# Kernel tuning notes

Hardware: AMD Instinct MI355X
Metric: run time of the kernel (lower is better)

## Reference

```python
import jax, jax.numpy as jnp
import numpy as np

ALPHA = 0.2  # LeakyReLU negative slope
EPS = 1e-16


def setup_inputs() -> dict:
    key = jax.random.key(0)
    k0, k1, k2, k3 = jax.random.split(key, 4)
    N, E, F_in, F_out, HEADS = 50000, 1600000, 256, 128, 4
    H = jax.random.normal(k0, (N, F_in), dtype=jnp.float32)
    edge_index = jax.random.randint(k1, (2, E), 0, N)  # row0=src, row1=dst
    # Xavier-ish scaled params
    W = jax.random.normal(k2, (HEADS, F_out, F_in), dtype=jnp.float32) * (1.0 / np.sqrt(F_in))
    a = jax.random.normal(k3, (HEADS, 2 * F_out), dtype=jnp.float32) * 0.1
    bias = jnp.zeros((F_out,), dtype=jnp.float32)
    return {"H": H, "edge_index": edge_index, "W": W, "a": a, "bias": bias}


def reference(H, edge_index, W, a, bias):
    """GAT layer: per-head edge attention + segment softmax over src + SpMM, mean over heads.

    H: [N, F_in]; edge_index: [2, E]; W: [heads, F_out, F_in]; a: [heads, 2*F_out]; bias: [F_out]
    Note: a(concat(h_src, h_dst)) == h_src @ a[:F_out] + h_dst @ a[F_out:], so we compute the
    two per-node scores once on nodes instead of materializing the E x 2*F_out concat.
    """
    N = H.shape[0]
    heads, F_out, _ = W.shape
    src, dst = edge_index[0], edge_index[1]
    outs = []
    for h in range(heads):
        Ht = H @ W[h].T                      # [N, F_out]
        s_src = Ht @ a[h, :F_out]            # [N]
        s_dst = Ht @ a[h, F_out:]            # [N]
        e = s_src[src] + s_dst[dst]          # [E]
        e = jnp.where(e > 0, e, ALPHA * e)   # LeakyReLU
        # segment softmax over src nodes (matches scatter amax + scatter_add)
        e_max = jax.ops.segment_max(e, src, num_segments=N)    # [N], -inf for isolated nodes
        e_exp = jnp.exp(e - e_max[src])                         # [E]
        denom = jax.ops.segment_sum(e_exp, src, num_segments=N) # [N]
        attn = e_exp / (denom[src] + EPS)                       # [E]
        # sparse.mm(attention, Ht): out[i] = sum_{(i,j) in E} attn_ij * Ht[j]
        out = jax.ops.segment_sum(attn[:, None] * Ht[dst], src, num_segments=N)  # [N, F_out]
        outs.append(out)
    final = jnp.mean(jnp.stack(outs, axis=0), axis=0) + bias
    return final
```

## Files before the change

kernel.cpp:

```cpp
#include <hip/hip_runtime.h>

#define ALPHA 0.2f
#define EPS 1e-16f

static constexpr int F_IN = 256;
static constexpr int F_OUT = 128;
static constexpr int HEADS = 4;
static constexpr int COLS = HEADS * F_OUT;

typedef __bf16 bf16x8 __attribute__((ext_vector_type(8)));
typedef float f32x4 __attribute__((ext_vector_type(4)));

static __device__ __forceinline__ unsigned short f2bf(float f) {
  unsigned int u = __float_as_uint(f);
  unsigned int r = (u + 0x7FFFu + ((u >> 16) & 1u)) >> 16;
  return (unsigned short)r;
}
static __device__ __forceinline__ float bf_lo(unsigned int u) {
  return __uint_as_float(u << 16);
}
static __device__ __forceinline__ float bf_hi(unsigned int u) {
  return __uint_as_float(u & 0xFFFF0000u);
}

__global__ __launch_bounds__(256) void k_wprep(const float* __restrict__ W,
                                               const float* __restrict__ a,
                                               unsigned short* __restrict__ Wb,
                                               float* __restrict__ u) {
  if (blockIdx.x < 128) {
    const int i = blockIdx.x * 256 + threadIdx.x;
    const float4 v = ((const float4*)W)[i];
    ((ushort4*)Wb)[i] = make_ushort4(f2bf(v.x), f2bf(v.y), f2bf(v.z), f2bf(v.w));
  } else {
    const int b = blockIdx.x - 128;
    const int h = b >> 1, dual = b & 1;
    const int k = threadIdx.x;
    float s = 0.f;
    for (int f = 0; f < F_OUT; ++f)
      s = fmaf(a[h * 2 * F_OUT + dual * F_OUT + f], W[((size_t)h * F_OUT + f) * F_IN + k], s);
    u[b * F_IN + k] = s;
  }
}

__global__ __launch_bounds__(256) void k_pre(const float4* __restrict__ H4,
    const float* __restrict__ u, unsigned short* __restrict__ Hb,
    float4* __restrict__ ssrc4, unsigned char* __restrict__ rec, int N, int CB,
    const int* __restrict__ src, int* __restrict__ cnt,
    unsigned short* __restrict__ rank, int E) {
  if ((int)blockIdx.x >= CB) {
    int i = (blockIdx.x - CB) * 256 + threadIdx.x;
    const int stride = 1024 * 256;
    for (; i < E; i += stride) rank[i] = (unsigned short)atomicAdd(&cnt[src[i]], 1);
    return;
  }
  const int wv = threadIdx.x >> 6, lane = threadIdx.x & 63;
  const int n = ((int)blockIdx.x << 2) + wv;
  if (n >= N) return;
  const float4 hv = H4[(size_t)n * 64 + lane];
  *((ushort4*)(Hb + (size_t)n * F_IN) + lane) =
      make_ushort4(f2bf(hv.x), f2bf(hv.y), f2bf(hv.z), f2bf(hv.w));
  float p[8];
#pragma unroll
  for (int c = 0; c < 8; ++c) {
    const float4 uv = *(const float4*)&u[c * F_IN + (lane << 2)];
    p[c] = fmaf(hv.x, uv.x, fmaf(hv.y, uv.y, fmaf(hv.z, uv.z, hv.w * uv.w)));
  }
#pragma unroll
  for (int c = 0; c < 8; ++c)
#pragma unroll
    for (int m = 1; m < 64; m <<= 1) p[c] += __shfl_xor(p[c], m);
  if (lane == 0) {
    ssrc4[n] = make_float4(p[0], p[2], p[4], p[6]);
    *(float4*)&rec[(size_t)n * 32] = make_float4(p[1], p[3], p[5], p[7]);
  }
}

__global__ __launch_bounds__(256) void k_gemm_q(const unsigned short* __restrict__ A,
                                                const unsigned short* __restrict__ B,
                                                unsigned char* __restrict__ Hq,
                                                unsigned char* __restrict__ rec, int N) {
  __shared__ __bf16 As[128][40];
  __shared__ __bf16 Bs[128][40];
  const int T = gridDim.x;
  const int q8 = T >> 3, r8 = T & 7;
  const int xcd = blockIdx.x & 7, ii = blockIdx.x >> 3;
  const int gp = (xcd < r8) ? xcd * (q8 + 1) + ii
                            : r8 * (q8 + 1) + (xcd - r8) * q8 + ii;
  const int by = gp >> 2;
  const int bx = gp & 3;
  const int t = threadIdx.x;
  const int w = t >> 6, l = t & 63;
  const int wr = w >> 1, wc = w & 1;
  const int m0 = by << 7, n0 = bx << 7;
  const int lr = t >> 1, seg16 = (t & 1) << 4;
  f32x4 acc[4][4] = {};
  for (int k0 = 0; k0 < F_IN; k0 += 32) {
    int ar = m0 + lr; if (ar >= N) ar = N - 1;
    const uint4 a0 = *(const uint4*)&A[(size_t)ar * F_IN + k0 + seg16];
    const uint4 a1 = *(const uint4*)&A[(size_t)ar * F_IN + k0 + seg16 + 8];
    const uint4 b0 = *(const uint4*)&B[(size_t)(n0 + lr) * F_IN + k0 + seg16];
    const uint4 b1 = *(const uint4*)&B[(size_t)(n0 + lr) * F_IN + k0 + seg16 + 8];
    __syncthreads();
    *(uint4*)&As[lr][seg16] = a0;  *(uint4*)&As[lr][seg16 + 8] = a1;
    *(uint4*)&Bs[lr][seg16] = b0;  *(uint4*)&Bs[lr][seg16 + 8] = b1;
    __syncthreads();
    const int kb = (l >> 4) << 3;
    bf16x8 af[4], bf_[4];
#pragma unroll
    for (int mi = 0; mi < 4; ++mi)
      af[mi] = *(const bf16x8*)&As[(wr << 6) + (mi << 4) + (l & 15)][kb];
#pragma unroll
    for (int ni = 0; ni < 4; ++ni)
      bf_[ni] = *(const bf16x8*)&Bs[(wc << 6) + (ni << 4) + (l & 15)][kb];
#pragma unroll
    for (int mi = 0; mi < 4; ++mi)
#pragma unroll
      for (int ni = 0; ni < 4; ++ni)
        acc[mi][ni] = __builtin_amdgcn_mfma_f32_16x16x32_bf16(af[mi], bf_[ni], acc[mi][ni], 0, 0, 0);
  }
  const int bxg = (bx << 1) + wc;
#pragma unroll
  for (int mi = 0; mi < 4; ++mi)
#pragma unroll
    for (int r = 0; r < 4; ++r) {
      float mx = 0.f;
#pragma unroll
      for (int ni = 0; ni < 4; ++ni) mx = fmaxf(mx, fabsf(acc[mi][ni][r]));
#pragma unroll
      for (int m = 1; m < 16; m <<= 1) mx = fmaxf(mx, __shfl_xor(mx, m));
      const int row = m0 + (wr << 6) + (mi << 4) + ((l >> 4) << 2) + r;
      if (row < N) {
        const float inv = (mx > 0.f) ? 127.f / mx : 0.f;
        if ((l & 15) == 0)
          *(unsigned short*)&rec[(size_t)row * 32 + 16 + (bxg << 1)] = f2bf(mx * (1.f / 127.f));
        unsigned int pk = 0;
#pragma unroll
        for (int ni = 0; ni < 4; ++ni) {
          float tq = fminf(fmaxf(rintf(acc[mi][ni][r] * inv), -127.f), 127.f);
          pk |= ((unsigned int)(((int)tq + 128) & 255)) << (8 * ni);
        }
        *(unsigned int*)&Hq[(size_t)row * 512 + (bxg << 6) + ((l & 15) << 2)] = pk;
      }
    }
}

__global__ __launch_bounds__(1024) void k_scan1(int* __restrict__ cnt,
                                                int* __restrict__ bsum, int N) {
  __shared__ int ws[16];
  const int t = threadIdx.x, g = blockIdx.x * 1024 + t;
  const int lane = t & 63, w = t >> 6;
  int v = (g < N) ? cnt[g] : 0;
#pragma unroll
  for (int o = 1; o < 64; o <<= 1) {
    const int y = __shfl_up(v, o);
    if (lane >= o) v += y;
  }
  if (lane == 63) ws[w] = v;
  __syncthreads();
  if (w == 0) {
    int s = (lane < 16) ? ws[lane] : 0;
#pragma unroll
    for (int o = 1; o < 16; o <<= 1) {
      const int y = __shfl_up(s, o);
      if (lane >= o) s += y;
    }
    if (lane < 16) ws[lane] = s;
  }
  __syncthreads();
  v += (w > 0) ? ws[w - 1] : 0;
  if (g < N) cnt[g] = v;
  if (t == 1023) bsum[blockIdx.x] = v;
}

__global__ __launch_bounds__(1024) void k_scan3(const int* __restrict__ part,
                                                const int* __restrict__ bsum,
                                                int* __restrict__ off, int N, int nb) {
  __shared__ int sbuf[256];
  const int t = threadIdx.x;
  if (t < 64) {
    int carry = 0;
    for (int base = 0; base < nb; base += 64) {
      int v = (base + t < nb) ? bsum[base + t] : 0;
#pragma unroll
      for (int o = 1; o < 64; o <<= 1) {
        const int y = __shfl_up(v, o);
        if (t >= o) v += y;
      }
      v += carry;
      if (base + t < nb) sbuf[base + t] = v;
      carry = __shfl(v, 63);
    }
  }
  __syncthreads();
  const int g = blockIdx.x * 1024 + t;
  if (g == 0) off[0] = 0;
  if (g < N) off[g + 1] = part[g] + (blockIdx.x ? sbuf[blockIdx.x - 1] : 0);
}

__global__ void k_scatter(const int* __restrict__ src, const int* __restrict__ dst,
                          const int* __restrict__ off, const unsigned short* __restrict__ rank,
                          unsigned short* __restrict__ csr_dst, int E) {
  int i = blockIdx.x * blockDim.x + threadIdx.x;
  const int stride = gridDim.x * blockDim.x;
  for (; i < E; i += stride)
    csr_dst[off[src[i]] + rank[i]] = (unsigned short)dst[i];
}

__global__ __launch_bounds__(256) void k_spmm(const uint2* __restrict__ Hq2,
    const float4* __restrict__ ssrc4, const unsigned char* __restrict__ rec,
    const int* __restrict__ off, const unsigned short* __restrict__ csr_dst,
    const float* __restrict__ bias, float* __restrict__ out, int N) {
  __shared__ float wbuf[4][8][72];
  __shared__ int   ibuf[4][64];
  const int wv = threadIdx.x >> 6;
  const int lane = threadIdx.x & 63;
  const int n = (blockIdx.x << 2) + wv;
  if (n >= N) return;
  const int hg = lane >> 4;
  const int b8 = lane >> 3;
  const float4 ss4 = ssrc4[n];
  float den4[4] = {};
  float acc[8] = {};
  float sw = 0.f;
  const int beg = off[n], end = off[n + 1];
  for (int c0 = beg; c0 < end; c0 += 64) {
    const int cnt = min(64, end - c0);
    if (lane < cnt) {
      const int d = csr_dst[c0 + lane];
      ibuf[wv][lane] = d << 6;
      const float4 sd4 = *(const float4*)&rec[(size_t)d * 32];
      const uint4  sc  = *(const uint4*)&rec[(size_t)d * 32 + 16];
      float e0 = ss4.x + sd4.x; e0 = fmaxf(e0, ALPHA * e0);
      float e1 = ss4.y + sd4.y; e1 = fmaxf(e1, ALPHA * e1);
      float e2 = ss4.z + sd4.z; e2 = fmaxf(e2, ALPHA * e2);
      float e3 = ss4.w + sd4.w; e3 = fmaxf(e3, ALPHA * e3);
      const float w0 = __expf(e0), w1 = __expf(e1), w2 = __expf(e2), w3 = __expf(e3);
      den4[0] += w0; den4[1] += w1; den4[2] += w2; den4[3] += w3;
      wbuf[wv][0][lane] = w0 * bf_lo(sc.x); wbuf[wv][1][lane] = w0 * bf_hi(sc.x);
      wbuf[wv][2][lane] = w1 * bf_lo(sc.y); wbuf[wv][3][lane] = w1 * bf_hi(sc.y);
      wbuf[wv][4][lane] = w2 * bf_lo(sc.z); wbuf[wv][5][lane] = w2 * bf_hi(sc.z);
      wbuf[wv][6][lane] = w3 * bf_lo(sc.w); wbuf[wv][7][lane] = w3 * bf_hi(sc.w);
    }
#pragma unroll 8
    for (int j = 0; j < cnt; ++j) {
      const float wgt = wbuf[wv][b8][j];
      const int db = ibuf[wv][j];
      const uint2 q = Hq2[db + lane];
      sw += wgt;
      acc[0] = fmaf(wgt, (float)(q.x & 0xffu),         acc[0]);
      acc[1] = fmaf(wgt, (float)((q.x >> 8) & 0xffu),  acc[1]);
      acc[2] = fmaf(wgt, (float)((q.x >> 16) & 0xffu), acc[2]);
      acc[3] = fmaf(wgt, (float)(q.x >> 24),           acc[3]);
      acc[4] = fmaf(wgt, (float)(q.y & 0xffu),         acc[4]);
      acc[5] = fmaf(wgt, (float)((q.y >> 8) & 0xffu),  acc[5]);
      acc[6] = fmaf(wgt, (float)((q.y >> 16) & 0xffu), acc[6]);
      acc[7] = fmaf(wgt, (float)(q.y >> 24),           acc[7]);
    }
  }
#pragma unroll
  for (int k = 0; k < 4; ++k)
#pragma unroll
    for (int m = 1; m < 64; m <<= 1) den4[k] += __shfl_xor(den4[k], m);
  const float r = 1.f / (den4[hg] + EPS);
  const float corr = 128.f * sw;
#pragma unroll
  for (int i = 0; i < 8; ++i) acc[i] = (acc[i] - corr) * r;
#pragma unroll
  for (int i = 0; i < 8; ++i) {
    acc[i] += __shfl_xor(acc[i], 16);
    acc[i] += __shfl_xor(acc[i], 32);
  }
  if (lane < 16) {
    const int base = ((lane >> 3) & 1) * 64 + ((lane & 7) << 1);
#pragma unroll
    for (int k = 0; k < 4; ++k) {
      const float2 b2 = *(const float2*)&bias[base + k * 16];
      *(float2*)&out[(size_t)n * F_OUT + base + k * 16] =
          make_float2(0.25f * acc[k] + b2.x, 0.25f * acc[k + 4] + b2.y);
    }
  }
}

extern "C" void kernel_launch(void* const* d_in, const int* in_sizes, int n_in,
                              void* d_out, int out_size, void* d_ws, size_t ws_size,
                              hipStream_t stream) {
  const float* H    = (const float*)d_in[0];
  const int*   ei   = (const int*)d_in[1];
  const float* W    = (const float*)d_in[2];
  const float* a    = (const float*)d_in[3];
  const float* bias = (const float*)d_in[4];
  const int N = in_sizes[0] / F_IN;
  const int E = in_sizes[1] / 2;
  const int* src = ei;
  const int* dst = ei + E;

  char* ws = (char*)d_ws;
  size_t o = 0;
  auto alloc = [&](size_t bytes) -> void* {
    void* p = ws + o;
    o = (o + bytes + 255) & ~(size_t)255;
    return p;
  };
  unsigned short* Hb  = (unsigned short*)alloc((size_t)N * F_IN * 2);
  unsigned short* Wb  = (unsigned short*)alloc((size_t)COLS * F_IN * 2);
  unsigned char*  Hq  = (unsigned char*)alloc((size_t)N * COLS);
  float* uvec = (float*)alloc(8 * F_IN * sizeof(float));
  float* ssrc = (float*)alloc((size_t)N * HEADS * sizeof(float));
  unsigned char* rec = (unsigned char*)alloc((size_t)N * 32);
  int*   cnt  = (int*)alloc((size_t)N * sizeof(int));
  int*   off  = (int*)alloc(((size_t)N + 1) * sizeof(int));
  unsigned short* csr = (unsigned short*)alloc((size_t)E * sizeof(unsigned short));
  unsigned short* rank = (unsigned short*)alloc((size_t)E * sizeof(unsigned short));
  const int nb = (N + 1023) / 1024;
  int*   bsum = (int*)alloc((size_t)nb * sizeof(int));

  hipMemsetAsync(cnt, 0, (size_t)N * sizeof(int), stream);

  k_wprep<<<136, 256, 0, stream>>>(W, a, Wb, uvec);
  const int CB = (N + 3) / 4;
  k_pre<<<CB + 1024, 256, 0, stream>>>((const float4*)H, uvec, Hb,
                                       (float4*)ssrc, rec, N, CB,
                                       src, cnt, rank, E);
  const int nb128 = (N + 127) / 128;
  k_gemm_q<<<4 * nb128, 256, 0, stream>>>(Hb, Wb, Hq, rec, N);
  k_scan1<<<nb, 1024, 0, stream>>>(cnt, bsum, N);
  k_scan3<<<nb, 1024, 0, stream>>>(cnt, bsum, off, N, nb);
  k_scatter<<<1024, 256, 0, stream>>>(src, dst, off, rank, csr, E);
  k_spmm<<<(N + 3) / 4, 256, 0, stream>>>((const uint2*)Hq, (const float4*)ssrc,
                                          rec, off, csr, bias, (float*)d_out, N);
}
```

Before: 300.8 us.

## Fuse H bf16 cast and attention score dot-products into the GEMM kernel

Removes the separate pre-pass that cast H to bf16 and computed per-node attention scores through precomputed W^T a vectors. The GEMM now loads fp32 H directly, converts it to bf16 in registers, and computes the src and dst scores from the bf16-rounded accumulators using a cross-wave reduction in shared memory. This drops the Hb round trip and one pass over H. In exchange the scores now come from bf16 products rather than fp32, which slightly changes accuracy, and each GEMM block reads twice as many bytes of A, with H re-read once per column block.

```diff
diff --git a/kernel.cpp b/kernel.cpp
--- a/kernel.cpp
+++ b/kernel.cpp
@@ -23,64 +23,29 @@
   return __uint_as_float(u & 0xFFFF0000u);
 }
 
-__global__ __launch_bounds__(256) void k_wprep(const float* __restrict__ W,
-                                               const float* __restrict__ a,
-                                               unsigned short* __restrict__ Wb,
-                                               float* __restrict__ u) {
-  if (blockIdx.x < 128) {
-    const int i = blockIdx.x * 256 + threadIdx.x;
-    const float4 v = ((const float4*)W)[i];
-    ((ushort4*)Wb)[i] = make_ushort4(f2bf(v.x), f2bf(v.y), f2bf(v.z), f2bf(v.w));
-  } else {
-    const int b = blockIdx.x - 128;
-    const int h = b >> 1, dual = b & 1;
-    const int k = threadIdx.x;
-    float s = 0.f;
-    for (int f = 0; f < F_OUT; ++f)
-      s = fmaf(a[h * 2 * F_OUT + dual * F_OUT + f], W[((size_t)h * F_OUT + f) * F_IN + k], s);
-    u[b * F_IN + k] = s;
-  }
-}
-
-__global__ __launch_bounds__(256) void k_pre(const float4* __restrict__ H4,
-    const float* __restrict__ u, unsigned short* __restrict__ Hb,
-    float4* __restrict__ ssrc4, unsigned char* __restrict__ rec, int N, int CB,
-    const int* __restrict__ src, int* __restrict__ cnt,
-    unsigned short* __restrict__ rank, int E) {
-  if ((int)blockIdx.x >= CB) {
-    int i = (blockIdx.x - CB) * 256 + threadIdx.x;
-    const int stride = 1024 * 256;
-    for (; i < E; i += stride) rank[i] = (unsigned short)atomicAdd(&cnt[src[i]], 1);
-    return;
-  }
-  const int wv = threadIdx.x >> 6, lane = threadIdx.x & 63;
-  const int n = ((int)blockIdx.x << 2) + wv;
-  if (n >= N) return;
-  const float4 hv = H4[(size_t)n * 64 + lane];
-  *((ushort4*)(Hb + (size_t)n * F_IN) + lane) =
-      make_ushort4(f2bf(hv.x), f2bf(hv.y), f2bf(hv.z), f2bf(hv.w));
-  float p[8];
-#pragma unroll
-  for (int c = 0; c < 8; ++c) {
-    const float4 uv = *(const float4*)&u[c * F_IN + (lane << 2)];
-    p[c] = fmaf(hv.x, uv.x, fmaf(hv.y, uv.y, fmaf(hv.z, uv.z, hv.w * uv.w)));
-  }
-#pragma unroll
-  for (int c = 0; c < 8; ++c)
-#pragma unroll
-    for (int m = 1; m < 64; m <<= 1) p[c] += __shfl_xor(p[c], m);
-  if (lane == 0) {
-    ssrc4[n] = make_float4(p[0], p[2], p[4], p[6]);
-    *(float4*)&rec[(size_t)n * 32] = make_float4(p[1], p[3], p[5], p[7]);
-  }
-}
-
-__global__ __launch_bounds__(256) void k_gemm_q(const unsigned short* __restrict__ A,
+__global__ __launch_bounds__(256) void k_wcast(const float* __restrict__ W,
+                                               unsigned short* __restrict__ Wb) {
+  const int i = blockIdx.x * 256 + threadIdx.x;
+  const float4 v = ((const float4*)W)[i];
+  ((ushort4*)Wb)[i] = make_ushort4(f2bf(v.x), f2bf(v.y), f2bf(v.z), f2bf(v.w));
+}
+
+__global__ void k_rank(const int* __restrict__ src, int* __restrict__ cnt,
+                       unsigned short* __restrict__ rank, int E) {
+  int i = blockIdx.x * blockDim.x + threadIdx.x;
+  const int stride = gridDim.x * blockDim.x;
+  for (; i < E; i += stride) rank[i] = (unsigned short)atomicAdd(&cnt[src[i]], 1);
+}
+
+__global__ __launch_bounds__(256) void k_gemm_q(const float* __restrict__ A,
                                                 const unsigned short* __restrict__ B,
                                                 unsigned char* __restrict__ Hq,
-                                                unsigned char* __restrict__ rec, int N) {
+                                                unsigned char* __restrict__ rec,
+                                                float* __restrict__ ssrc,
+                                                const float* __restrict__ Av, int N) {
   __shared__ __bf16 As[128][40];
   __shared__ __bf16 Bs[128][40];
+  __shared__ float sS[128], sD[128];
   const int T = gridDim.x;
   const int q8 = T >> 3, r8 = T & 7;
   const int xcd = blockIdx.x & 7, ii = blockIdx.x >> 3;
@@ -96,13 +61,20 @@
   f32x4 acc[4][4] = {};
   for (int k0 = 0; k0 < F_IN; k0 += 32) {
     int ar = m0 + lr; if (ar >= N) ar = N - 1;
-    const uint4 a0 = *(const uint4*)&A[(size_t)ar * F_IN + k0 + seg16];
-    const uint4 a1 = *(const uint4*)&A[(size_t)ar * F_IN + k0 + seg16 + 8];
+    const float4 f0 = *(const float4*)&A[(size_t)ar * F_IN + k0 + seg16];
+    const float4 f1 = *(const float4*)&A[(size_t)ar * F_IN + k0 + seg16 + 4];
+    const float4 f2 = *(const float4*)&A[(size_t)ar * F_IN + k0 + seg16 + 8];
+    const float4 f3 = *(const float4*)&A[(size_t)ar * F_IN + k0 + seg16 + 12];
     const uint4 b0 = *(const uint4*)&B[(size_t)(n0 + lr) * F_IN + k0 + seg16];
     const uint4 b1 = *(const uint4*)&B[(size_t)(n0 + lr) * F_IN + k0 + seg16 + 8];
+    bf16x8 v0, v1;
+    v0[0] = (__bf16)f0.x; v0[1] = (__bf16)f0.y; v0[2] = (__bf16)f0.z; v0[3] = (__bf16)f0.w;
+    v0[4] = (__bf16)f1.x; v0[5] = (__bf16)f1.y; v0[6] = (__bf16)f1.z; v0[7] = (__bf16)f1.w;
+    v1[0] = (__bf16)f2.x; v1[1] = (__bf16)f2.y; v1[2] = (__bf16)f2.z; v1[3] = (__bf16)f2.w;
+    v1[4] = (__bf16)f3.x; v1[5] = (__bf16)f3.y; v1[6] = (__bf16)f3.z; v1[7] = (__bf16)f3.w;
     __syncthreads();
-    *(uint4*)&As[lr][seg16] = a0;  *(uint4*)&As[lr][seg16 + 8] = a1;
-    *(uint4*)&Bs[lr][seg16] = b0;  *(uint4*)&Bs[lr][seg16 + 8] = b1;
+    *(bf16x8*)&As[lr][seg16] = v0;  *(bf16x8*)&As[lr][seg16 + 8] = v1;
+    *(uint4*)&Bs[lr][seg16] = b0;   *(uint4*)&Bs[lr][seg16 + 8] = b1;
     __syncthreads();
     const int kb = (l >> 4) << 3;
     bf16x8 af[4], bf_[4];
@@ -117,6 +89,62 @@
 #pragma unroll
       for (int ni = 0; ni < 4; ++ni)
         acc[mi][ni] = __builtin_amdgcn_mfma_f32_16x16x32_bf16(af[mi], bf_[ni], acc[mi][ni], 0, 0, 0);
+  }
+  {
+    float as_[4], ad_[4];
+#pragma unroll
+    for (int ni = 0; ni < 4; ++ni) {
+      const int f = (wc << 6) + (ni << 4) + (l & 15);
+      as_[ni] = Av[bx * 256 + f];
+      ad_[ni] = Av[bx * 256 + 128 + f];
+    }
+#pragma unroll
+    for (int mi = 0; mi < 4; ++mi)
+#pragma unroll
+      for (int r = 0; r < 4; ++r) {
+        float ds_ = 0.f, dd_ = 0.f;
+#pragma unroll
+        for (int ni = 0; ni < 4; ++ni) {
+          ds_ = fmaf(acc[mi][ni][r], as_[ni], ds_);
+          dd_ = fmaf(acc[mi][ni][r], ad_[ni], dd_);
+        }
+#pragma unroll
+        for (int m = 1; m < 16; m <<= 1) {
+          ds_ += __shfl_xor(ds_, m);
+          dd_ += __shfl_xor(dd_, m);
+        }
+        if (wc == 0 && (l & 15) == 0) {
+          const int rl = (wr << 6) + (mi << 4) + ((l >> 4) << 2) + r;
+          sS[rl] = ds_; sD[rl] = dd_;
+        }
+      }
+    __syncthreads();
+    if (wc == 1) {
+#pragma unroll
+      for (int mi = 0; mi < 4; ++mi)
+#pragma unroll
+        for (int r = 0; r < 4; ++r) {
+          float ds_ = 0.f, dd_ = 0.f;
+#pragma unroll
+          for (int ni = 0; ni < 4; ++ni) {
+            ds_ = fmaf(acc[mi][ni][r], as_[ni], ds_);
+            dd_ = fmaf(acc[mi][ni][r], ad_[ni], dd_);
+          }
+#pragma unroll
+          for (int m = 1; m < 16; m <<= 1) {
+            ds_ += __shfl_xor(ds_, m);
+            dd_ += __shfl_xor(dd_, m);
+          }
+          if ((l & 15) == 0) {
+            const int rl = (wr << 6) + (mi << 4) + ((l >> 4) << 2) + r;
+            const int row = m0 + rl;
+            if (row < N) {
+              ssrc[row * 4 + bx] = sS[rl] + ds_;
+              *(float*)&rec[(size_t)row * 32 + (bx << 2)] = sD[rl] + dd_;
+            }
+          }
+        }
+    }
   }
   const int bxg = (bx << 1) + wc;
 #pragma unroll
@@ -301,10 +329,8 @@
     o = (o + bytes + 255) & ~(size_t)255;
     return p;
   };
-  unsigned short* Hb  = (unsigned short*)alloc((size_t)N * F_IN * 2);
   unsigned short* Wb  = (unsigned short*)alloc((size_t)COLS * F_IN * 2);
   unsigned char*  Hq  = (unsigned char*)alloc((size_t)N * COLS);
-  float* uvec = (float*)alloc(8 * F_IN * sizeof(float));
   float* ssrc = (float*)alloc((size_t)N * HEADS * sizeof(float));
   unsigned char* rec = (unsigned char*)alloc((size_t)N * 32);
   int*   cnt  = (int*)alloc((size_t)N * sizeof(int));
@@ -316,13 +342,10 @@
 
   hipMemsetAsync(cnt, 0, (size_t)N * sizeof(int), stream);
 
-  k_wprep<<<136, 256, 0, stream>>>(W, a, Wb, uvec);
-  const int CB = (N + 3) / 4;
-  k_pre<<<CB + 1024, 256, 0, stream>>>((const float4*)H, uvec, Hb,
-                                       (float4*)ssrc, rec, N, CB,
-                                       src, cnt, rank, E);
+  k_wcast<<<128, 256, 0, stream>>>(W, Wb);
+  k_rank<<<1024, 256, 0, stream>>>(src, cnt, rank, E);
   const int nb128 = (N + 127) / 128;
-  k_gemm_q<<<4 * nb128, 256, 0, stream>>>(Hb, Wb, Hq, rec, N);
+  k_gemm_q<<<4 * nb128, 256, 0, stream>>>(H, Wb, Hq, rec, ssrc, a, N);
   k_scan1<<<nb, 1024, 0, stream>>>(cnt, bsum, N);
   k_scan3<<<nb, 1024, 0, stream>>>(cnt, bsum, off, N, nb);
   k_scatter<<<1024, 256, 0, stream>>>(src, dst, off, rank, csr, E);
```

Result: no change. 301.3 us (+0.2%).
